# Kernel tuning notes

Measured on AMD Instinct MI355X. Metric: run time of the kernel, lower is better.

The kernel has to match this reference:

```python
import jax, jax.numpy as jnp
import numpy as np

B, N, D, R, E = 512, 32, 300, 5, 256
V_SENSE, V_GLOBAL = 20000, 50000  # last_idx_senses, last_idx_globals - last_idx_senses


def setup_inputs() -> dict:
    key = jax.random.key(0)
    ks = jax.random.split(key, 10)
    x = jax.random.normal(ks[0], (B, N, D), jnp.float32)
    edge_index = jax.random.randint(ks[1], (B, 2, E), 0, N)
    edge_type = jnp.sort(jax.random.randint(ks[2], (B, E), 0, R), axis=-1)
    # parameters (xavier-ish scales)
    conv_W = jax.random.normal(ks[3], (R, D, D), jnp.float32) * np.float32(1.0 / np.sqrt(D))
    W0 = jax.random.normal(ks[4], (D, D), jnp.float32) * np.float32(np.sqrt(2.0 / (D + D)))
    update_gate = jnp.ones((1,), jnp.float32)
    glob_W = jax.random.normal(ks[5], (V_GLOBAL, D), jnp.float32) * np.float32(1.0 / np.sqrt(D))
    glob_b = jnp.zeros((V_GLOBAL,), jnp.float32)
    sense_W = jax.random.normal(ks[6], (V_SENSE, D), jnp.float32) * np.float32(1.0 / np.sqrt(D))
    sense_b = jnp.zeros((V_SENSE,), jnp.float32)
    memory0 = jnp.zeros((N, D), jnp.float32)  # initial persisted memory (zeros vector broadcast)
    return dict(x=x, edge_index=edge_index, edge_type=edge_type, conv_W=conv_W, W0=W0,
                update_gate=update_gate, glob_W=glob_W, glob_b=glob_b,
                sense_W=sense_W, sense_b=sense_b, memory0=memory0)


def reference(x, edge_index, edge_type, conv_W, W0, update_gate, glob_W, glob_b, sense_W, sense_b, memory0):
    R_ = conv_W.shape[0]
    N_ = x.shape[1]

    def step(mem, inp):
        xs, ei, et = inp                      # [N,D], [2,E], [E]
        src, dst = ei[0], ei[1]
        # per-relation transformed features (GCNConv, bias=False)
        xw = jnp.einsum('nd,rde->rne', xs, conv_W)          # [R,N,D]
        # per-relation degrees with self-loops (PyG GCNConv symmetric norm)
        onehot = jax.nn.one_hot(et, R_, dtype=xs.dtype)     # [E,R]
        deg = 1.0 + jax.ops.segment_sum(onehot, dst, num_segments=N_)  # [N,R]
        dinv = jax.lax.rsqrt(deg)                           # [N,R]
        coeff = dinv[src, et] * dinv[dst, et]               # [E]
        msg = coeff[:, None] * xw[et, src]                  # [E,D]
        agg = jax.ops.segment_sum(msg, dst, num_segments=N_)  # sum over relations' convs
        self_term = jnp.einsum('rnd,nr->nd', xw, dinv * dinv)  # self-loop of each GCNConv
        composite = agg + self_term
        # prevlayer_connection = eye(N) @ (x @ W_0) = x @ W_0
        proposed = composite + xs @ W0
        new_mem = update_gate * proposed + (1.0 - update_gate) * mem  # rgcn_conv, persisted
        x1 = jax.nn.relu(new_mem)[0]                        # current node features [D]
        return new_mem, x1

    _, x1_all = jax.lax.scan(step, memory0, (x, edge_index, edge_type))  # [B,D]
    logits_g = x1_all @ glob_W.T + glob_b                   # [B,V_GLOBAL]
    logits_s = x1_all @ sense_W.T + sense_b                 # [B,V_SENSE]
    return (jax.nn.log_softmax(logits_g, axis=-1), jax.nn.log_softmax(logits_s, axis=-1))
```

## Files before the change

### kernel.cpp

```cpp
#include <hip/hip_runtime.h>
#include <stdint.h>

#define BDIM   512
#define NNODE  32
#define DDIM   300
#define NREL   5
#define NEDGE  256
#define VGLOB  50000
#define VSENSE 20000

#define K1PAD  1856
#define K2PAD  320
#define TG_GLOB  391
#define TG_SENSE 157
#define TGTOT  548
#define GROWS  50048
#define SROWS  20096
#define WROWS  70144
#define NCHUNK 3
#define KCH    10
#define NSCH   16
#define SCHL   32

#define NB_W2  21920
#define NB_Z   512
#define NB_W   2784

typedef __attribute__((ext_vector_type(8))) short short8;
typedef __attribute__((ext_vector_type(4))) float f32x4;

__device__ __forceinline__ unsigned short f2bf(float x) {
    unsigned int u = __float_as_uint(x);
    u += 0x7fffu + ((u >> 16) & 1u);
    return (unsigned short)(u >> 16);
}

__device__ __forceinline__ float powi(float x, int n) {
    float r = 1.f, p = x;
    while (n) { if (n & 1) r *= p; p *= p; n >>= 1; }
    return r;
}

#define AS1 __attribute__((address_space(1)))
#define AS3 __attribute__((address_space(3)))
__device__ __forceinline__ void gload16(const void* gp, void* lp) {
    __builtin_amdgcn_global_load_lds((AS1 void*)gp, (AS3 void*)lp, 16, 0, 0);
}

__global__ __launch_bounds__(256) void k_prep_all(
    const float* __restrict__ x, const int* __restrict__ ei,
    const int* __restrict__ et, unsigned short* __restrict__ Zb,
    const float* __restrict__ convW, const float* __restrict__ W0f,
    unsigned short* __restrict__ Wcb,
    const float* __restrict__ globW, const float* __restrict__ senseW,
    unsigned short* __restrict__ Wgb, int zbase)
{
    int blk = blockIdx.x, t = threadIdx.x;

    if (blk < zbase) {
        int idx = blk * 256 + t;
        int row = idx / 80, kq = (idx - row * 80) * 4;
        unsigned int p0 = 0, p1 = 0;
        if (kq < DDIM) {
            const float* srcp = nullptr;
            if (row < GROWS) { if (row < VGLOB) srcp = globW + (size_t)row * DDIM; }
            else { int sr = row - GROWS; if (sr < VSENSE) srcp = senseW + (size_t)sr * DDIM; }
            if (srcp) {
                float4 v = *(const float4*)(srcp + kq);
                p0 = (unsigned int)f2bf(v.x) | ((unsigned int)f2bf(v.y) << 16);
                p1 = (unsigned int)f2bf(v.z) | ((unsigned int)f2bf(v.w) << 16);
            }
        }
        uint2 pp; pp.x = p0; pp.y = p1;
        *(uint2*)(Wgb + (size_t)row * K2PAD + kq) = pp;
        return;
    }

    if (blk < zbase + NB_Z) {
        int b = blk - zbase;
        __shared__ int   cnt[NNODE * NREL];
        __shared__ float dinv[NNODE * NREL];
        __shared__ int   ssrc[NEDGE];
        __shared__ int   sdst[NEDGE];
        __shared__ int   setp[NEDGE];
        __shared__ float z[6][DDIM];

        const int* src = ei + (size_t)b * 2 * NEDGE;
        const int* dst = src + NEDGE;
        const int* etb = et + (size_t)b * NEDGE;

        if (t < NNODE * NREL) cnt[t] = 0;
        __syncthreads();
        if (t < NEDGE) {
            int s = src[t], d = dst[t], r = etb[t];
            ssrc[t] = s; sdst[t] = d; setp[t] = r;
            atomicAdd(&cnt[d * NREL + r], 1);
        }
        __syncthreads();
        if (t < NNODE * NREL) dinv[t] = rsqrtf(1.0f + (float)cnt[t]);
        __syncthreads();

        const float* xb = x + (size_t)b * NNODE * DDIM;
        for (int d = t; d < DDIM; d += 256) {
            float x0 = xb[d];
#pragma unroll
            for (int r = 0; r < NREL; r++) { float c = dinv[r]; z[r][d] = c * c * x0; }
            z[5][d] = x0;
        }
        __syncthreads();
        for (int e = 0; e < NEDGE; e++) {
            if (sdst[e] != 0) continue;
            int s = ssrc[e], r = setp[e];
            float coeff = dinv[s * NREL + r] * dinv[r];
            const float* xs = xb + (size_t)s * DDIM;
            for (int d = t; d < DDIM; d += 256) z[r][d] += coeff * xs[d];
        }
        __syncthreads();
        unsigned short* zo = Zb + (size_t)b * K1PAD;
        for (int k = t; k < K1PAD; k += 256) {
            unsigned short v = 0;
            if (k < 6 * DDIM) { int r = k / DDIM, d = k - r * DDIM; v = f2bf(z[r][d]); }
            zo[k] = v;
        }
        return;
    }

    {
        int idx = (blk - zbase - NB_Z) * 256 + t;
        if (idx >= 384 * K1PAD) return;
        int n = idx / K1PAD, k = idx - n * K1PAD;
        float v = 0.f;
        if (n < DDIM && k < 6 * DDIM) {
            int r = k / DDIM, d = k - r * DDIM;
            v = (r < NREL) ? convW[((size_t)r * DDIM + d) * DDIM + n]
                           : W0f[(size_t)d * DDIM + n];
        }
        Wcb[idx] = f2bf(v);
    }
}

template<int MODE>
__global__ __launch_bounds__(256) void k_gemm_b(
    const unsigned short* __restrict__ A, int ldk, int nk, int kchunk,
    int tiles0,
    const unsigned short* __restrict__ B0, int ldb0,
    const float* __restrict__ bias0, float* __restrict__ C0, long ldc0,
    int nstore0, int tilebase0,
    const unsigned short* __restrict__ B1, int ldb1,
    const float* __restrict__ bias1, float* __restrict__ C1, long ldc1,
    int nstore1, int tilebase1,
    float* __restrict__ pmax, float* __restrict__ psum)
{
    __shared__ __align__(16) char Alds[128 * 128];
    __shared__ __align__(16) char Blds[128 * 128];

    int t = threadIdx.x;
    int tile, mrep;
    if constexpr (MODE == 0) {
        tile = blockIdx.x; mrep = blockIdx.y;
    } else {
        int i = blockIdx.x + TGTOT * blockIdx.y;
        if (i < 2176) { int g = i >> 5, r = i & 31; tile = g * 8 + (r & 7); mrep = r >> 3; }
        else          { int j = i - 2176; tile = 544 + (j & 3); mrep = j >> 2; }
    }

    const unsigned short* Bp; const float* bias; float* Cout;
    long ldc; int ldb, nstore, tileidx, tloc;
    if (tile < tiles0) {
        Bp = B0; bias = bias0; Cout = C0; ldc = ldc0;
        ldb = ldb0; nstore = nstore0; tloc = tile; tileidx = tilebase0 + tile;
    } else {
        tloc = tile - tiles0;
        Bp = B1; bias = bias1; Cout = C1; ldc = ldc1;
        ldb = ldb1; nstore = nstore1; tileidx = tilebase1 + tloc;
    }
    int n0 = tloc * 128;
    int m0 = mrep * 128;

    int kt_lo = 0, kt_hi = nk >> 6;
    if constexpr (MODE == 0) {
        if (kchunk > 0) {
            kt_lo = blockIdx.z * kchunk;
            int hi = kt_lo + kchunk;
            if (hi < kt_hi) kt_hi = hi;
            Cout += (size_t)blockIdx.z * (BDIM * 304);
        }
    }

    int lane = t & 63, wid = t >> 6;
    int wm = wid >> 1, wn = wid & 1;
    int l15 = lane & 15, lq = lane >> 4;

    int trow = t >> 3;
    int sb = ((t & 7) << 4) ^ ((trow & 7) << 4);
    const char* Ag = (const char*)A + (size_t)(m0 + trow) * (ldk * 2) + sb;
    const char* Bg = (const char*)Bp + (size_t)(n0 + trow) * (ldb * 2) + sb;
    char* Al = Alds + t * 16;
    char* Bl = Blds + t * 16;
    size_t a32 = (size_t)32 * (ldk * 2);
    size_t b32 = (size_t)32 * (ldb * 2);

    int sw = (l15 & 7) << 4;
    int aoff0 = (lq * 16) ^ sw;
    int aoff1 = (64 + lq * 16) ^ sw;
    const char* Arow = Alds + (wm * 64 + l15) * 128;
    const char* Brow = Blds + (wn * 64 + l15) * 128;

    f32x4 acc[4][4] = {};

    for (int kt = kt_lo; kt < kt_hi; ++kt) {
        int k0b = kt << 7;
        const char* Agk = Ag + k0b;
        const char* Bgk = Bg + k0b;
#pragma unroll
        for (int c = 0; c < 4; c++) {
            gload16(Agk + c * a32, Al + c * 4096);
            gload16(Bgk + c * b32, Bl + c * 4096);
        }
        __syncthreads();
        short8 afr[4][2], bfr[4][2];
#pragma unroll
        for (int i = 0; i < 4; i++) {
            const char* Ab = Arow + i * (16 * 128);
            const char* Bb = Brow + i * (16 * 128);
            afr[i][0] = *(const short8*)(Ab + aoff0);
            afr[i][1] = *(const short8*)(Ab + aoff1);
            bfr[i][0] = *(const short8*)(Bb + aoff0);
            bfr[i][1] = *(const short8*)(Bb + aoff1);
        }
#pragma unroll
        for (int ks = 0; ks < 2; ks++)
#pragma unroll
            for (int mi = 0; mi < 4; mi++)
#pragma unroll
                for (int ni = 0; ni < 4; ni++)
                    acc[mi][ni] = __builtin_amdgcn_mfma_f32_16x16x32_bf16(
                        afr[mi][ks], bfr[ni][ks], acc[mi][ni], 0, 0, 0);
        __syncthreads();
    }

    if constexpr (MODE == 1) {
        __shared__ float sMax[128][2];
        __shared__ float sSum[128][2];
#pragma unroll
        for (int mi = 0; mi < 4; mi++) {
            int row = m0 + wm * 64 + mi * 16 + lq * 4;
#pragma unroll
            for (int r = 0; r < 4; r++) {
                float vals[4];
                float rowmax = -3.0e38f;
#pragma unroll
                for (int ni = 0; ni < 4; ni++) {
                    int col = n0 + wn * 64 + ni * 16 + l15;
                    float v = -3.0e38f;
                    if (col < nstore) v = acc[mi][ni][r] + bias[col];
                    vals[ni] = v;
                    rowmax = fmaxf(rowmax, v);
                }
#pragma unroll
                for (int ni = 0; ni < 4; ni++) {
                    int col = n0 + wn * 64 + ni * 16 + l15;
                    if (col < nstore) Cout[(size_t)(row + r) * ldc + col] = vals[ni];
                }
#pragma unroll
                for (int off = 1; off < 16; off <<= 1)
                    rowmax = fmaxf(rowmax, __shfl_xor(rowmax, off, 64));
                float s = 0.f;
#pragma unroll
                for (int ni = 0; ni < 4; ni++) s += __expf(vals[ni] - rowmax);
#pragma unroll
                for (int off = 1; off < 16; off <<= 1) s += __shfl_xor(s, off, 64);
                if (l15 == 0) {
                    int rl = wm * 64 + mi * 16 + lq * 4 + r;
                    sMax[rl][wn] = rowmax; sSum[rl][wn] = s;
                }
            }
        }
        __syncthreads();
        if (t < 128) {
            float ma = sMax[t][0], mb = sMax[t][1];
            float M = fmaxf(ma, mb);
            float S = sSum[t][0] * __expf(ma - M) + sSum[t][1] * __expf(mb - M);
            size_t o = (size_t)tileidx * BDIM + (m0 + t);
            pmax[o] = M; psum[o] = S;
        }
    } else {
#pragma unroll
        for (int mi = 0; mi < 4; mi++) {
            int row = m0 + wm * 64 + mi * 16 + lq * 4;
#pragma unroll
            for (int ni = 0; ni < 4; ni++) {
                int col = n0 + wn * 64 + ni * 16 + l15;
                if (col < nstore) {
#pragma unroll
                    for (int r = 0; r < 4; r++)
                        Cout[(size_t)(row + r) * ldc + col] = acc[mi][ni][r];
                }
            }
        }
    }
}

__global__ __launch_bounds__(256) void k_gemm_f32(
    const unsigned short* __restrict__ A, int ldk, int nk,
    int tiles0,
    const float* __restrict__ B0, int ldb0, int ksrc0, int brows0,
    const float* __restrict__ bias0, float* __restrict__ C0, long ldc0,
    int nstore0, int tilebase0,
    const float* __restrict__ B1, int ldb1, int ksrc1, int brows1,
    const float* __restrict__ bias1, float* __restrict__ C1, long ldc1,
    int nstore1, int tilebase1,
    float* __restrict__ pmax, float* __restrict__ psum)
{
    __shared__ __align__(16) short Alds[128 * 32];
    __shared__ __align__(16) short Blds[128 * 32];

    int t = threadIdx.x;
    int bx = blockIdx.x;
    const float* Bsrc; const float* bias; float* Cout;
    long ldc; int ldb, ksrc, brows, nstore, tileidx;
    if (bx < tiles0) {
        Bsrc = B0; bias = bias0; Cout = C0; ldc = ldc0;
        ldb = ldb0; ksrc = ksrc0; brows = brows0; nstore = nstore0;
        tileidx = tilebase0 + bx;
    } else {
        bx -= tiles0;
        Bsrc = B1; bias = bias1; Cout = C1; ldc = ldc1;
        ldb = ldb1; ksrc = ksrc1; brows = brows1; nstore = nstore1;
        tileidx = tilebase1 + bx;
    }
    int n0 = bx * 128;
    int m0 = blockIdx.y * 128;

    int lane = t & 63, wid = t >> 6;
    int wm = wid >> 1, wn = wid & 1;
    int l15 = lane & 15, lq = lane >> 4;

    f32x4 acc[4][4] = {};

    int arow = t >> 1, acol = (t & 1) * 16;
    const unsigned short* aptr = A + (size_t)(m0 + arow) * ldk + acol;
    int brow = t >> 3, bkq = (t & 7) * 4;

    int kt_hi = nk / 32;
    for (int kt = 0; kt < kt_hi; ++kt) {
        int k0 = kt * 32;
        uint4 a0 = *(const uint4*)(aptr + k0);
        uint4 a1 = *(const uint4*)(aptr + k0 + 8);
        float4 bv[4];
#pragma unroll
        for (int j = 0; j < 4; j++) {
            int row = n0 + brow + 32 * j;
            float4 v = {0.f, 0.f, 0.f, 0.f};
            if (row < brows && (k0 + bkq + 4) <= ksrc)
                v = *(const float4*)(Bsrc + (size_t)row * ldb + k0 + bkq);
            bv[j] = v;
        }
        __syncthreads();
        *(uint4*)&Alds[arow * 32 + acol] = a0;
        *(uint4*)&Alds[arow * 32 + acol + 8] = a1;
#pragma unroll
        for (int j = 0; j < 4; j++) {
            unsigned int p0 = (unsigned int)f2bf(bv[j].x) | ((unsigned int)f2bf(bv[j].y) << 16);
            unsigned int p1 = (unsigned int)f2bf(bv[j].z) | ((unsigned int)f2bf(bv[j].w) << 16);
            uint2 pp; pp.x = p0; pp.y = p1;
            *(uint2*)&Blds[(brow + 32 * j) * 32 + bkq] = pp;
        }
        __syncthreads();
        short8 afr[4], bfr[4];
#pragma unroll
        for (int i = 0; i < 4; i++) {
            afr[i] = *(const short8*)&Alds[(wm * 64 + i * 16 + l15) * 32 + lq * 8];
            bfr[i] = *(const short8*)&Blds[(wn * 64 + i * 16 + l15) * 32 + lq * 8];
        }
#pragma unroll
        for (int mi = 0; mi < 4; mi++)
#pragma unroll
            for (int ni = 0; ni < 4; ni++)
                acc[mi][ni] = __builtin_amdgcn_mfma_f32_16x16x32_bf16(
                    afr[mi], bfr[ni], acc[mi][ni], 0, 0, 0);
    }

    __shared__ float sMax[128][2];
    __shared__ float sSum[128][2];
#pragma unroll
    for (int mi = 0; mi < 4; mi++) {
        int row = m0 + wm * 64 + mi * 16 + lq * 4;
#pragma unroll
        for (int r = 0; r < 4; r++) {
            float vals[4];
            float rowmax = -3.0e38f;
#pragma unroll
            for (int ni = 0; ni < 4; ni++) {
                int col = n0 + wn * 64 + ni * 16 + l15;
                float v = -3.0e38f;
                if (col < nstore) v = acc[mi][ni][r] + bias[col];
                vals[ni] = v;
                rowmax = fmaxf(rowmax, v);
            }
#pragma unroll
            for (int ni = 0; ni < 4; ni++) {
                int col = n0 + wn * 64 + ni * 16 + l15;
                if (col < nstore) Cout[(size_t)(row + r) * ldc + col] = vals[ni];
            }
#pragma unroll
            for (int off = 1; off < 16; off <<= 1)
                rowmax = fmaxf(rowmax, __shfl_xor(rowmax, off, 64));
            float s = 0.f;
#pragma unroll
            for (int ni = 0; ni < 4; ni++) s += __expf(vals[ni] - rowmax);
#pragma unroll
            for (int off = 1; off < 16; off <<= 1) s += __shfl_xor(s, off, 64);
            if (l15 == 0) {
                int rl = wm * 64 + mi * 16 + lq * 4 + r;
                sMax[rl][wn] = rowmax; sSum[rl][wn] = s;
            }
        }
    }
    __syncthreads();
    if (t < 128) {
        float ma = sMax[t][0], mb = sMax[t][1];
        float M = fmaxf(ma, mb);
        float S = sSum[t][0] * __expf(ma - M) + sSum[t][1] * __expf(mb - M);
        size_t o = (size_t)tileidx * BDIM + (m0 + t);
        pmax[o] = M; psum[o] = S;
    }
}

__global__ __launch_bounds__(320) void k_scan_local(
    const float* __restrict__ prop, float* __restrict__ scanA,
    const float* __restrict__ gate)
{
    int d = threadIdx.x; if (d >= 304) return;
    int blk = blockIdx.x;
    float g = gate[0], og = 1.f - g;
    float m = 0.f;
    const float* p0 = prop + (size_t)blk * SCHL * 304 + d;
    const float* p1 = p0 + (size_t)BDIM * 304;
    const float* p2 = p1 + (size_t)BDIM * 304;
    float* o = scanA + (size_t)blk * SCHL * 304 + d;
#pragma unroll
    for (int i = 0; i < SCHL; i++) {
        size_t off = (size_t)i * 304;
        float pv = p0[off] + p1[off] + p2[off];
        m = g * pv + og * m;
        o[off] = m;
    }
}

__global__ __launch_bounds__(320) void k_finalize_x1(
    const float* __restrict__ scanA, const float* __restrict__ mem0,
    const float* __restrict__ gate, unsigned short* __restrict__ x1b)
{
    int b = blockIdx.x, d = threadIdx.x;
    unsigned short v = 0;
    if (d < DDIM) {
        float g = gate[0], og = 1.f - g;
        float cS = powi(og, SCHL);
        int chunk = b >> 5;
        float m = mem0[d];
        for (int c = 0; c < chunk; c++)
            m = scanA[(size_t)(c * SCHL + SCHL - 1) * 304 + d] + cS * m;
        float mval = scanA[(size_t)b * 304 + d]
                   + powi(og, (b & (SCHL - 1)) + 1) * m;
        v = f2bf(fmaxf(mval, 0.f));
    }
    if (d < K2PAD) x1b[(size_t)b * K2PAD + d] = v;
}

__global__ __launch_bounds__(256) void k_lse_fix(
    const float* __restrict__ pmax, const float* __restrict__ psum,
    float* __restrict__ out)
{
    int b = blockIdx.x, seg = blockIdx.y, t = threadIdx.x;
    int base = seg ? TG_GLOB : 0;
    int nt = seg ? TG_SENSE : TG_GLOB;
    float M = -3.0e38f, S = 0.f;
    for (int i = t; i < nt; i += 256) {
        size_t o = (size_t)(base + i) * BDIM + b;
        float m = pmax[o], s = psum[o];
        if (m > M) { S = S * __expf(M - m) + s; M = m; }
        else       { S += s * __expf(m - M); }
    }
#pragma unroll
    for (int off = 1; off < 64; off <<= 1) {
        float Mo = __shfl_xor(M, off, 64), So = __shfl_xor(S, off, 64);
        float Mn = fmaxf(M, Mo);
        S = S * __expf(M - Mn) + So * __expf(Mo - Mn);
        M = Mn;
    }
    __shared__ float sM[4], sS[4];
    __shared__ float sL;
    int lane = t & 63, wid = t >> 6;
    if (lane == 0) { sM[wid] = M; sS[wid] = S; }
    __syncthreads();
    if (t == 0) {
        M = sM[0]; S = sS[0];
#pragma unroll
        for (int w = 1; w < 4; w++) {
            float Mo = sM[w], So = sS[w];
            float Mn = fmaxf(M, Mo);
            S = S * __expf(M - Mn) + So * __expf(Mo - Mn);
            M = Mn;
        }
        sL = M + __logf(S);
    }
    __syncthreads();
    float L = sL;
    float* row = seg ? out + (size_t)BDIM * VGLOB + (size_t)b * VSENSE
                     : out + (size_t)b * VGLOB;
    int n4 = (seg ? VSENSE : VGLOB) >> 2;
    float4* r4 = (float4*)row;
    for (int i = t; i < n4; i += 256) {
        float4 v = r4[i];
        v.x -= L; v.y -= L; v.z -= L; v.w -= L;
        r4[i] = v;
    }
}

extern "C" void kernel_launch(void* const* d_in, const int* in_sizes, int n_in,
                              void* d_out, int out_size, void* d_ws, size_t ws_size,
                              hipStream_t stream)
{
    (void)in_sizes; (void)n_in; (void)out_size;
    const float* x      = (const float*)d_in[0];
    const int*   ei     = (const int*)d_in[1];
    const int*   et     = (const int*)d_in[2];
    const float* convW  = (const float*)d_in[3];
    const float* W0f    = (const float*)d_in[4];
    const float* gate   = (const float*)d_in[5];
    const float* globW  = (const float*)d_in[6];
    const float* globB  = (const float*)d_in[7];
    const float* senseW = (const float*)d_in[8];
    const float* senseB = (const float*)d_in[9];
    const float* mem0   = (const float*)d_in[10];
    float* out = (float*)d_out;

    char* w = (char*)d_ws;
    unsigned short* Zb  = (unsigned short*)(w + 0);
    unsigned short* Wcb = (unsigned short*)(w + 1900544);
    unsigned short* x1b = (unsigned short*)(w + 3325952);
    float* prop         = (float*)(w + 3653632);
    float* scanA        = (float*)(w + 5521408);
    float* pmax         = (float*)(w + 6144000);
    float* psum         = (float*)(w + 7266304);
    unsigned short* Wgb = (unsigned short*)(w + 8388608);
    const size_t WS_NEED_BIG = 8388608 + (size_t)WROWS * K2PAD * 2;
    bool bigws = ws_size >= WS_NEED_BIG;

    int zbase = bigws ? NB_W2 : 0;
    int nprep = zbase + NB_Z + NB_W;
    k_prep_all<<<nprep, 256, 0, stream>>>(x, ei, et, Zb, convW, W0f, Wcb,
                                          globW, senseW, Wgb, zbase);

    k_gemm_b<0><<<dim3(3, 4, NCHUNK), 256, 0, stream>>>(Zb, K1PAD, K1PAD, KCH,
        3, Wcb, K1PAD, nullptr, prop, 304, 304, 0,
        nullptr, 0, nullptr, nullptr, 0, 0, 0,
        nullptr, nullptr);

    k_scan_local<<<NSCH, 320, 0, stream>>>(prop, scanA, gate);
    k_finalize_x1<<<BDIM, 320, 0, stream>>>(scanA, mem0, gate, x1b);

    if (bigws) {
        const unsigned short* WgbS = Wgb + (size_t)GROWS * K2PAD;
        k_gemm_b<1><<<dim3(TGTOT, 4), 256, 0, stream>>>(x1b, K2PAD, K2PAD, 0,
            TG_GLOB, Wgb, K2PAD, globB, out, VGLOB, VGLOB, 0,
            WgbS, K2PAD, senseB, out + (size_t)BDIM * VGLOB, VSENSE, VSENSE, TG_GLOB,
            pmax, psum);
    } else {
        k_gemm_f32<<<dim3(TGTOT, 4), 256, 0, stream>>>(x1b, K2PAD, K2PAD,
            TG_GLOB, globW, DDIM, DDIM, VGLOB, globB, out, VGLOB, VGLOB, 0,
            senseW, DDIM, DDIM, VSENSE, senseB, out + (size_t)BDIM * VGLOB, VSENSE, VSENSE, TG_GLOB,
            pmax, psum);
    }
    k_lse_fix<<<dim3(BDIM, 2), 256, 0, stream>>>(pmax, psum, out);
}
```

Baseline: 389.6 us.

## Double-buffer GEMMs, fuse middle stages into cooperative kernel, widen weight conversion

Both bf16 GEMMs now use double-buffered LDS, so the next K-tile is prefetched while MFMAs run on the current one, with a combined waitcnt+barrier per step. The stage-1 GEMM, chunked scan and finalize kernels are merged into one cooperative launch that uses grid syncs, falling back to three separate kernels if the cooperative launch fails. The weight bf16 conversion now has each thread handle 16 elements with 16-byte stores, which cuts the block count. This removes launch overhead and exposed load latency, at the cost of doubled LDS use and grid-sync costs on a small 128-block grid.

```diff
diff --git a/kernel.cpp b/kernel.cpp
--- a/kernel.cpp
+++ b/kernel.cpp
@@ -1,4 +1,5 @@
 #include <hip/hip_runtime.h>
+#include <hip/hip_cooperative_groups.h>
 #include <stdint.h>
 
 #define BDIM   512
@@ -22,7 +23,7 @@
 #define NSCH   16
 #define SCHL   32
 
-#define NB_W2  21920
+#define NB_W2  5480
 #define NB_Z   512
 #define NB_W   2784
 
@@ -46,6 +47,8 @@
 __device__ __forceinline__ void gload16(const void* gp, void* lp) {
     __builtin_amdgcn_global_load_lds((AS1 void*)gp, (AS3 void*)lp, 16, 0, 0);
 }
+
+#define WAIT_BARRIER() asm volatile("s_waitcnt vmcnt(0) lgkmcnt(0)\n\ts_barrier" ::: "memory")
 
 __global__ __launch_bounds__(256) void k_prep_all(
     const float* __restrict__ x, const int* __restrict__ ei,
@@ -59,20 +62,26 @@
 
     if (blk < zbase) {
         int idx = blk * 256 + t;
-        int row = idx / 80, kq = (idx - row * 80) * 4;
-        unsigned int p0 = 0, p1 = 0;
-        if (kq < DDIM) {
-            const float* srcp = nullptr;
-            if (row < GROWS) { if (row < VGLOB) srcp = globW + (size_t)row * DDIM; }
-            else { int sr = row - GROWS; if (sr < VSENSE) srcp = senseW + (size_t)sr * DDIM; }
-            if (srcp) {
+        int row = idx / 20, q0 = (idx - row * 20) * 4;
+        const float* srcp = nullptr;
+        if (row < GROWS) { if (row < VGLOB) srcp = globW + (size_t)row * DDIM; }
+        else { int sr = row - GROWS; if (sr < VSENSE) srcp = senseW + (size_t)sr * DDIM; }
+        unsigned int pk[8];
+#pragma unroll
+        for (int j = 0; j < 4; j++) {
+            int kq = (q0 + j) * 4;
+            unsigned int p0 = 0, p1 = 0;
+            if (srcp && kq < DDIM) {
                 float4 v = *(const float4*)(srcp + kq);
                 p0 = (unsigned int)f2bf(v.x) | ((unsigned int)f2bf(v.y) << 16);
                 p1 = (unsigned int)f2bf(v.z) | ((unsigned int)f2bf(v.w) << 16);
             }
-        }
-        uint2 pp; pp.x = p0; pp.y = p1;
-        *(uint2*)(Wgb + (size_t)row * K2PAD + kq) = pp;
+            pk[2 * j] = p0; pk[2 * j + 1] = p1;
+        }
+        uint4* dst = (uint4*)(Wgb + (size_t)row * K2PAD + q0 * 4);
+        uint4 u0; u0.x = pk[0]; u0.y = pk[1]; u0.z = pk[2]; u0.w = pk[3];
+        uint4 u1; u1.x = pk[4]; u1.y = pk[5]; u1.z = pk[6]; u1.w = pk[7];
+        dst[0] = u0; dst[1] = u1;
         return;
     }
 
@@ -139,53 +148,18 @@
     }
 }
 
-template<int MODE>
-__global__ __launch_bounds__(256) void k_gemm_b(
-    const unsigned short* __restrict__ A, int ldk, int nk, int kchunk,
-    int tiles0,
-    const unsigned short* __restrict__ B0, int ldb0,
-    const float* __restrict__ bias0, float* __restrict__ C0, long ldc0,
-    int nstore0, int tilebase0,
-    const unsigned short* __restrict__ B1, int ldb1,
-    const float* __restrict__ bias1, float* __restrict__ C1, long ldc1,
-    int nstore1, int tilebase1,
-    float* __restrict__ pmax, float* __restrict__ psum)
-{
-    __shared__ __align__(16) char Alds[128 * 128];
-    __shared__ __align__(16) char Blds[128 * 128];
-
-    int t = threadIdx.x;
-    int tile, mrep;
-    if constexpr (MODE == 0) {
-        tile = blockIdx.x; mrep = blockIdx.y;
-    } else {
-        int i = blockIdx.x + TGTOT * blockIdx.y;
-        if (i < 2176) { int g = i >> 5, r = i & 31; tile = g * 8 + (r & 7); mrep = r >> 3; }
-        else          { int j = i - 2176; tile = 544 + (j & 3); mrep = j >> 2; }
-    }
-
-    const unsigned short* Bp; const float* bias; float* Cout;
-    long ldc; int ldb, nstore, tileidx, tloc;
-    if (tile < tiles0) {
-        Bp = B0; bias = bias0; Cout = C0; ldc = ldc0;
-        ldb = ldb0; nstore = nstore0; tloc = tile; tileidx = tilebase0 + tile;
-    } else {
-        tloc = tile - tiles0;
-        Bp = B1; bias = bias1; Cout = C1; ldc = ldc1;
-        ldb = ldb1; nstore = nstore1; tileidx = tilebase1 + tloc;
-    }
-    int n0 = tloc * 128;
-    int m0 = mrep * 128;
-
-    int kt_lo = 0, kt_hi = nk >> 6;
-    if constexpr (MODE == 0) {
-        if (kchunk > 0) {
-            kt_lo = blockIdx.z * kchunk;
-            int hi = kt_lo + kchunk;
-            if (hi < kt_hi) kt_hi = hi;
-            Cout += (size_t)blockIdx.z * (BDIM * 304);
-        }
-    }
+__device__ __forceinline__ void stage1_tile(
+    int nt, int mt, int z, const unsigned short* __restrict__ Zb,
+    const unsigned short* __restrict__ Wcb, float* __restrict__ prop, int t)
+{
+    __shared__ __align__(16) char Alds[2][16384];
+    __shared__ __align__(16) char Blds[2][16384];
+
+    int m0 = mt * 128, n0 = nt * 128;
+    int kt_lo = z * KCH;
+    int kt_hi = kt_lo + KCH; if (kt_hi > 29) kt_hi = 29;
+    int nst = kt_hi - kt_lo;
+    float* Cout = prop + (size_t)z * (BDIM * 304);
 
     int lane = t & 63, wid = t >> 6;
     int wm = wid >> 1, wn = wid & 1;
@@ -193,40 +167,47 @@
 
     int trow = t >> 3;
     int sb = ((t & 7) << 4) ^ ((trow & 7) << 4);
-    const char* Ag = (const char*)A + (size_t)(m0 + trow) * (ldk * 2) + sb;
-    const char* Bg = (const char*)Bp + (size_t)(n0 + trow) * (ldb * 2) + sb;
-    char* Al = Alds + t * 16;
-    char* Bl = Blds + t * 16;
-    size_t a32 = (size_t)32 * (ldk * 2);
-    size_t b32 = (size_t)32 * (ldb * 2);
+    const char* Ag = (const char*)Zb + (size_t)(m0 + trow) * (K1PAD * 2) + sb
+                   + ((size_t)kt_lo << 7);
+    const char* Bg = (const char*)Wcb + (size_t)(n0 + trow) * (K1PAD * 2) + sb
+                   + ((size_t)kt_lo << 7);
+    const size_t a32 = (size_t)32 * (K1PAD * 2);
 
     int sw = (l15 & 7) << 4;
     int aoff0 = (lq * 16) ^ sw;
     int aoff1 = (64 + lq * 16) ^ sw;
-    const char* Arow = Alds + (wm * 64 + l15) * 128;
-    const char* Brow = Blds + (wn * 64 + l15) * 128;
 
     f32x4 acc[4][4] = {};
 
-    for (int kt = kt_lo; kt < kt_hi; ++kt) {
-        int k0b = kt << 7;
-        const char* Agk = Ag + k0b;
-        const char* Bgk = Bg + k0b;
-#pragma unroll
-        for (int c = 0; c < 4; c++) {
-            gload16(Agk + c * a32, Al + c * 4096);
-            gload16(Bgk + c * b32, Bl + c * 4096);
-        }
-        __syncthreads();
+#pragma unroll
+    for (int c = 0; c < 4; c++) {
+        gload16(Ag + c * a32, Alds[0] + t * 16 + c * 4096);
+        gload16(Bg + c * a32, Blds[0] + t * 16 + c * 4096);
+    }
+    WAIT_BARRIER();
+
+    for (int s = 0; s < nst; ++s) {
+        int cur = s & 1;
+        if (s + 1 < nst) {
+            const char* Agk = Ag + ((size_t)(s + 1) << 7);
+            const char* Bgk = Bg + ((size_t)(s + 1) << 7);
+#pragma unroll
+            for (int c = 0; c < 4; c++) {
+                gload16(Agk + c * a32, Alds[cur ^ 1] + t * 16 + c * 4096);
+                gload16(Bgk + c * a32, Blds[cur ^ 1] + t * 16 + c * 4096);
+            }
+        }
+        const char* Arow = Alds[cur] + (wm * 64 + l15) * 128;
+        const char* Brow = Blds[cur] + (wn * 64 + l15) * 128;
         short8 afr[4][2], bfr[4][2];
 #pragma unroll
-        for (int i = 0; i < 4; i++) {
-            const char* Ab = Arow + i * (16 * 128);
-            const char* Bb = Brow + i * (16 * 128);
-            afr[i][0] = *(const short8*)(Ab + aoff0);
-            afr[i][1] = *(const short8*)(Ab + aoff1);
-            bfr[i][0] = *(const short8*)(Bb + aoff0);
-            bfr[i][1] = *(const short8*)(Bb + aoff1);
+        for (int ii = 0; ii < 4; ii++) {
+            const char* Ab = Arow + ii * (16 * 128);
+            const char* Bb = Brow + ii * (16 * 128);
+            afr[ii][0] = *(const short8*)(Ab + aoff0);
+            afr[ii][1] = *(const short8*)(Ab + aoff1);
+            bfr[ii][0] = *(const short8*)(Bb + aoff0);
+            bfr[ii][1] = *(const short8*)(Bb + aoff1);
         }
 #pragma unroll
         for (int ks = 0; ks < 2; ks++)
@@ -236,68 +217,232 @@
                 for (int ni = 0; ni < 4; ni++)
                     acc[mi][ni] = __builtin_amdgcn_mfma_f32_16x16x32_bf16(
                         afr[mi][ks], bfr[ni][ks], acc[mi][ni], 0, 0, 0);
-        __syncthreads();
-    }
-
-    if constexpr (MODE == 1) {
-        __shared__ float sMax[128][2];
-        __shared__ float sSum[128][2];
-#pragma unroll
-        for (int mi = 0; mi < 4; mi++) {
-            int row = m0 + wm * 64 + mi * 16 + lq * 4;
-#pragma unroll
-            for (int r = 0; r < 4; r++) {
-                float vals[4];
-                float rowmax = -3.0e38f;
-#pragma unroll
-                for (int ni = 0; ni < 4; ni++) {
-                    int col = n0 + wn * 64 + ni * 16 + l15;
-                    float v = -3.0e38f;
-                    if (col < nstore) v = acc[mi][ni][r] + bias[col];
-                    vals[ni] = v;
-                    rowmax = fmaxf(rowmax, v);
-                }
-#pragma unroll
-                for (int ni = 0; ni < 4; ni++) {
-                    int col = n0 + wn * 64 + ni * 16 + l15;
-                    if (col < nstore) Cout[(size_t)(row + r) * ldc + col] = vals[ni];
-                }
-#pragma unroll
-                for (int off = 1; off < 16; off <<= 1)
-                    rowmax = fmaxf(rowmax, __shfl_xor(rowmax, off, 64));
-                float s = 0.f;
-#pragma unroll
-                for (int ni = 0; ni < 4; ni++) s += __expf(vals[ni] - rowmax);
-#pragma unroll
-                for (int off = 1; off < 16; off <<= 1) s += __shfl_xor(s, off, 64);
-                if (l15 == 0) {
-                    int rl = wm * 64 + mi * 16 + lq * 4 + r;
-                    sMax[rl][wn] = rowmax; sSum[rl][wn] = s;
-                }
-            }
-        }
-        __syncthreads();
-        if (t < 128) {
-            float ma = sMax[t][0], mb = sMax[t][1];
-            float M = fmaxf(ma, mb);
-            float S = sSum[t][0] * __expf(ma - M) + sSum[t][1] * __expf(mb - M);
-            size_t o = (size_t)tileidx * BDIM + (m0 + t);
-            pmax[o] = M; psum[o] = S;
-        }
+        WAIT_BARRIER();
+    }
+
+#pragma unroll
+    for (int mi = 0; mi < 4; mi++) {
+        int row = m0 + wm * 64 + mi * 16 + lq * 4;
+#pragma unroll
+        for (int ni = 0; ni < 4; ni++) {
+            int col = n0 + wn * 64 + ni * 16 + l15;
+            if (col < 304) {
+#pragma unroll
+                for (int r = 0; r < 4; r++)
+                    Cout[(size_t)(row + r) * 304 + col] = acc[mi][ni][r];
+            }
+        }
+    }
+}
+
+__device__ __forceinline__ void scan_chunk(
+    int blk, const float* __restrict__ prop, float* __restrict__ scanA,
+    const float* __restrict__ gate, int t)
+{
+    float g = gate[0], og = 1.f - g;
+    for (int d = t; d < 304; d += 256) {
+        float m = 0.f;
+        const float* p0 = prop + (size_t)blk * SCHL * 304 + d;
+        const float* p1 = p0 + (size_t)BDIM * 304;
+        const float* p2 = p1 + (size_t)BDIM * 304;
+        float* o = scanA + (size_t)blk * SCHL * 304 + d;
+#pragma unroll
+        for (int i = 0; i < SCHL; i++) {
+            size_t off = (size_t)i * 304;
+            float pv = p0[off] + p1[off] + p2[off];
+            m = g * pv + og * m;
+            o[off] = m;
+        }
+    }
+}
+
+__device__ __forceinline__ void finalize_b(
+    int b, const float* __restrict__ scanA, const float* __restrict__ mem0,
+    const float* __restrict__ gate, unsigned short* __restrict__ x1b, int t)
+{
+    float g = gate[0], og = 1.f - g;
+    float cS = powi(og, SCHL);
+    int chunk = b >> 5;
+    for (int d = t; d < K2PAD; d += 256) {
+        unsigned short v = 0;
+        if (d < DDIM) {
+            float m = mem0[d];
+            for (int c = 0; c < chunk; c++)
+                m = scanA[(size_t)(c * SCHL + SCHL - 1) * 304 + d] + cS * m;
+            float mval = scanA[(size_t)b * 304 + d]
+                       + powi(og, (b & (SCHL - 1)) + 1) * m;
+            v = f2bf(fmaxf(mval, 0.f));
+        }
+        x1b[(size_t)b * K2PAD + d] = v;
+    }
+}
+
+__global__ __launch_bounds__(256) void k_mid_coop(
+    const unsigned short* __restrict__ Zb, const unsigned short* __restrict__ Wcb,
+    float* __restrict__ prop, const float* __restrict__ gate,
+    const float* __restrict__ mem0, float* __restrict__ scanA,
+    unsigned short* __restrict__ x1b)
+{
+    int blk = blockIdx.x, t = threadIdx.x;
+    if (blk < 36) {
+        int nt = blk % 3, mt = (blk / 3) & 3, z = blk / 12;
+        stage1_tile(nt, mt, z, Zb, Wcb, prop, t);
+    }
+    cooperative_groups::this_grid().sync();
+    if (blk < NSCH) scan_chunk(blk, prop, scanA, gate, t);
+    cooperative_groups::this_grid().sync();
+#pragma unroll
+    for (int j = 0; j < 4; j++)
+        finalize_b(blk + 128 * j, scanA, mem0, gate, x1b, t);
+}
+
+__global__ __launch_bounds__(256) void k_stage1(
+    const unsigned short* __restrict__ Zb, const unsigned short* __restrict__ Wcb,
+    float* __restrict__ prop)
+{
+    stage1_tile(blockIdx.x, blockIdx.y, blockIdx.z, Zb, Wcb, prop, threadIdx.x);
+}
+__global__ __launch_bounds__(256) void k_scan(
+    const float* __restrict__ prop, float* __restrict__ scanA,
+    const float* __restrict__ gate)
+{
+    scan_chunk(blockIdx.x, prop, scanA, gate, threadIdx.x);
+}
+__global__ __launch_bounds__(256) void k_fin(
+    const float* __restrict__ scanA, const float* __restrict__ mem0,
+    const float* __restrict__ gate, unsigned short* __restrict__ x1b)
+{
+    finalize_b(blockIdx.x, scanA, mem0, gate, x1b, threadIdx.x);
+}
+
+__global__ __launch_bounds__(256) void k_gemm_stats(
+    const unsigned short* __restrict__ A,
+    const unsigned short* __restrict__ Wgb,
+    const float* __restrict__ globB, const float* __restrict__ senseB,
+    float* __restrict__ out,
+    float* __restrict__ pmax, float* __restrict__ psum)
+{
+    __shared__ __align__(16) char Alds[2][16384];
+    __shared__ __align__(16) char Blds[2][16384];
+    __shared__ float sMax[128][2];
+    __shared__ float sSum[128][2];
+
+    int t = threadIdx.x;
+    int i = blockIdx.x + TGTOT * blockIdx.y;
+    int tile, mrep;
+    if (i < 2176) { int g = i >> 5, r = i & 31; tile = g * 8 + (r & 7); mrep = r >> 3; }
+    else          { int j = i - 2176; tile = 544 + (j & 3); mrep = j >> 2; }
+
+    const float* bias; float* Cout; long ldc; int nstore, tloc;
+    if (tile < TG_GLOB) {
+        bias = globB; Cout = out; ldc = VGLOB; nstore = VGLOB; tloc = tile;
     } else {
-#pragma unroll
-        for (int mi = 0; mi < 4; mi++) {
-            int row = m0 + wm * 64 + mi * 16 + lq * 4;
+        tloc = tile - TG_GLOB;
+        bias = senseB; Cout = out + (size_t)BDIM * VGLOB; ldc = VSENSE; nstore = VSENSE;
+    }
+    int n0 = tloc * 128;
+    int m0 = mrep * 128;
+    const unsigned short* Bp = Wgb + (size_t)tile * 128 * K2PAD;
+
+    int lane = t & 63, wid = t >> 6;
+    int wm = wid >> 1, wn = wid & 1;
+    int l15 = lane & 15, lq = lane >> 4;
+
+    int trow = t >> 3;
+    int sb = ((t & 7) << 4) ^ ((trow & 7) << 4);
+    const char* Ag = (const char*)A + (size_t)(m0 + trow) * (K2PAD * 2) + sb;
+    const char* Bg = (const char*)Bp + (size_t)trow * (K2PAD * 2) + sb;
+    const size_t a32 = (size_t)32 * (K2PAD * 2);
+
+    int sw = (l15 & 7) << 4;
+    int aoff0 = (lq * 16) ^ sw;
+    int aoff1 = (64 + lq * 16) ^ sw;
+
+    f32x4 acc[4][4] = {};
+
+#pragma unroll
+    for (int c = 0; c < 4; c++) {
+        gload16(Ag + c * a32, Alds[0] + t * 16 + c * 4096);
+        gload16(Bg + c * a32, Blds[0] + t * 16 + c * 4096);
+    }
+    WAIT_BARRIER();
+
+#pragma unroll
+    for (int kt = 0; kt < 5; ++kt) {
+        int cur = kt & 1;
+        if (kt < 4) {
+            const char* Agk = Ag + ((size_t)(kt + 1) << 7);
+            const char* Bgk = Bg + ((size_t)(kt + 1) << 7);
+#pragma unroll
+            for (int c = 0; c < 4; c++) {
+                gload16(Agk + c * a32, Alds[cur ^ 1] + t * 16 + c * 4096);
+                gload16(Bgk + c * a32, Blds[cur ^ 1] + t * 16 + c * 4096);
+            }
+        }
+        const char* Arow = Alds[cur] + (wm * 64 + l15) * 128;
+        const char* Brow = Blds[cur] + (wn * 64 + l15) * 128;
+        short8 afr[4][2], bfr[4][2];
+#pragma unroll
+        for (int ii = 0; ii < 4; ii++) {
+            const char* Ab = Arow + ii * (16 * 128);
+            const char* Bb = Brow + ii * (16 * 128);
+            afr[ii][0] = *(const short8*)(Ab + aoff0);
+            afr[ii][1] = *(const short8*)(Ab + aoff1);
+            bfr[ii][0] = *(const short8*)(Bb + aoff0);
+            bfr[ii][1] = *(const short8*)(Bb + aoff1);
+        }
+#pragma unroll
+        for (int ks = 0; ks < 2; ks++)
+#pragma unroll
+            for (int mi = 0; mi < 4; mi++)
+#pragma unroll
+                for (int ni = 0; ni < 4; ni++)
+                    acc[mi][ni] = __builtin_amdgcn_mfma_f32_16x16x32_bf16(
+                        afr[mi][ks], bfr[ni][ks], acc[mi][ni], 0, 0, 0);
+        WAIT_BARRIER();
+    }
+
+#pragma unroll
+    for (int mi = 0; mi < 4; mi++) {
+        int row = m0 + wm * 64 + mi * 16 + lq * 4;
+#pragma unroll
+        for (int r = 0; r < 4; r++) {
+            float vals[4];
+            float rowmax = -3.0e38f;
 #pragma unroll
             for (int ni = 0; ni < 4; ni++) {
                 int col = n0 + wn * 64 + ni * 16 + l15;
-                if (col < nstore) {
-#pragma unroll
-                    for (int r = 0; r < 4; r++)
-                        Cout[(size_t)(row + r) * ldc + col] = acc[mi][ni][r];
-                }
-            }
-        }
+                float v = -3.0e38f;
+                if (col < nstore) v = acc[mi][ni][r] + bias[col];
+                vals[ni] = v;
+                rowmax = fmaxf(rowmax, v);
+            }
+#pragma unroll
+            for (int ni = 0; ni < 4; ni++) {
+                int col = n0 + wn * 64 + ni * 16 + l15;
+                if (col < nstore) Cout[(size_t)(row + r) * ldc + col] = vals[ni];
+            }
+#pragma unroll
+            for (int off = 1; off < 16; off <<= 1)
+                rowmax = fmaxf(rowmax, __shfl_xor(rowmax, off, 64));
+            float s = 0.f;
+#pragma unroll
+            for (int ni = 0; ni < 4; ni++) s += __expf(vals[ni] - rowmax);
+#pragma unroll
+            for (int off = 1; off < 16; off <<= 1) s += __shfl_xor(s, off, 64);
+            if (l15 == 0) {
+                int rl = wm * 64 + mi * 16 + lq * 4 + r;
+                sMax[rl][wn] = rowmax; sSum[rl][wn] = s;
+            }
+        }
+    }
+    __syncthreads();
+    if (t < 128) {
+        float ma = sMax[t][0], mb = sMax[t][1];
+        float M = fmaxf(ma, mb);
+        float S = sSum[t][0] * __expf(ma - M) + sSum[t][1] * __expf(mb - M);
+        size_t o = (size_t)tile * BDIM + (m0 + t);
+        pmax[o] = M; psum[o] = S;
     }
 }
 
@@ -369,9 +514,9 @@
         __syncthreads();
         short8 afr[4], bfr[4];
 #pragma unroll
-        for (int i = 0; i < 4; i++) {
-            afr[i] = *(const short8*)&Alds[(wm * 64 + i * 16 + l15) * 32 + lq * 8];
-            bfr[i] = *(const short8*)&Blds[(wn * 64 + i * 16 + l15) * 32 + lq * 8];
+        for (int ii = 0; ii < 4; ii++) {
+            afr[ii] = *(const short8*)&Alds[(wm * 64 + ii * 16 + l15) * 32 + lq * 8];
+            bfr[ii] = *(const short8*)&Blds[(wn * 64 + ii * 16 + l15) * 32 + lq * 8];
         }
 #pragma unroll
         for (int mi = 0; mi < 4; mi++)
@@ -425,47 +570,6 @@
         size_t o = (size_t)tileidx * BDIM + (m0 + t);
         pmax[o] = M; psum[o] = S;
     }
-}
-
-__global__ __launch_bounds__(320) void k_scan_local(
-    const float* __restrict__ prop, float* __restrict__ scanA,
-    const float* __restrict__ gate)
-{
-    int d = threadIdx.x; if (d >= 304) return;
-    int blk = blockIdx.x;
-    float g = gate[0], og = 1.f - g;
-    float m = 0.f;
-    const float* p0 = prop + (size_t)blk * SCHL * 304 + d;
-    const float* p1 = p0 + (size_t)BDIM * 304;
-    const float* p2 = p1 + (size_t)BDIM * 304;
-    float* o = scanA + (size_t)blk * SCHL * 304 + d;
-#pragma unroll
-    for (int i = 0; i < SCHL; i++) {
-        size_t off = (size_t)i * 304;
-        float pv = p0[off] + p1[off] + p2[off];
-        m = g * pv + og * m;
-        o[off] = m;
-    }
-}
-
-__global__ __launch_bounds__(320) void k_finalize_x1(
-    const float* __restrict__ scanA, const float* __restrict__ mem0,
-    const float* __restrict__ gate, unsigned short* __restrict__ x1b)
-{
-    int b = blockIdx.x, d = threadIdx.x;
-    unsigned short v = 0;
-    if (d < DDIM) {
-        float g = gate[0], og = 1.f - g;
-        float cS = powi(og, SCHL);
-        int chunk = b >> 5;
-        float m = mem0[d];
-        for (int c = 0; c < chunk; c++)
-            m = scanA[(size_t)(c * SCHL + SCHL - 1) * 304 + d] + cS * m;
-        float mval = scanA[(size_t)b * 304 + d]
-                   + powi(og, (b & (SCHL - 1)) + 1) * m;
-        v = f2bf(fmaxf(mval, 0.f));
-    }
-    if (d < K2PAD) x1b[(size_t)b * K2PAD + d] = v;
 }
 
 __global__ __launch_bounds__(256) void k_lse_fix(
@@ -553,20 +657,22 @@
     k_prep_all<<<nprep, 256, 0, stream>>>(x, ei, et, Zb, convW, W0f, Wcb,
                                           globW, senseW, Wgb, zbase);
 
-    k_gemm_b<0><<<dim3(3, 4, NCHUNK), 256, 0, stream>>>(Zb, K1PAD, K1PAD, KCH,
-        3, Wcb, K1PAD, nullptr, prop, 304, 304, 0,
-        nullptr, 0, nullptr, nullptr, 0, 0, 0,
-        nullptr, nullptr);
-
-    k_scan_local<<<NSCH, 320, 0, stream>>>(prop, scanA, gate);
-    k_finalize_x1<<<BDIM, 320, 0, stream>>>(scanA, mem0, gate, x1b);
+    {
+        void* margs[] = { (void*)&Zb, (void*)&Wcb, (void*)&prop, (void*)&gate,
+                          (void*)&mem0, (void*)&scanA, (void*)&x1b };
+        hipError_t ce = hipLaunchCooperativeKernel(
+            reinterpret_cast<void*>(k_mid_coop), dim3(128), dim3(256),
+            margs, 0, stream);
+        if (ce != hipSuccess) {
+            k_stage1<<<dim3(3, 4, NCHUNK), 256, 0, stream>>>(Zb, Wcb, prop);
+            k_scan<<<NSCH, 256, 0, stream>>>(prop, scanA, gate);
+            k_fin<<<BDIM, 256, 0, stream>>>(scanA, mem0, gate, x1b);
+        }
+    }
 
     if (bigws) {
-        const unsigned short* WgbS = Wgb + (size_t)GROWS * K2PAD;
-        k_gemm_b<1><<<dim3(TGTOT, 4), 256, 0, stream>>>(x1b, K2PAD, K2PAD, 0,
-            TG_GLOB, Wgb, K2PAD, globB, out, VGLOB, VGLOB, 0,
-            WgbS, K2PAD, senseB, out + (size_t)BDIM * VGLOB, VSENSE, VSENSE, TG_GLOB,
-            pmax, psum);
+        k_gemm_stats<<<dim3(TGTOT, 4), 256, 0, stream>>>(x1b, Wgb, globB, senseB,
+                                                         out, pmax, psum);
     } else {
         k_gemm_f32<<<dim3(TGTOT, 4), 256, 0, stream>>>(x1b, K2PAD, K2PAD,
             TG_GLOB, globW, DDIM, DDIM, VGLOB, globB, out, VGLOB, VGLOB, 0,
```

After: 477.9 us. +22.7%, slower.
